# Kernel tuning notes

Hardware: AMD Instinct MI355X
Metric: run time of the kernel (lower is better)

The kernel has to match this reference:

```python
import jax, jax.numpy as jnp
import numpy as np

N = 50000
EPS = 1e-5


def gcn_conv(x, W, b, src, dst, n):
    # x: [n, Cin]; W: [Cin, Cout]; src/dst: [E+n] with self-loops included
    h = x @ W  # dense GEMM
    deg = jax.ops.segment_sum(jnp.ones_like(dst, dtype=h.dtype), dst, num_segments=n)
    dinv = jnp.where(deg > 0, jax.lax.rsqrt(deg), 0.0)
    norm = dinv[src] * dinv[dst]  # [E+n]
    msgs = h[src] * norm[:, None]  # gather + scale
    out = jax.ops.segment_sum(msgs, dst, num_segments=n)  # scatter-add
    return out + b


def batch_norm(x, gamma, beta, mean, var):
    return (x - mean) * jax.lax.rsqrt(var + EPS) * gamma + beta


def setup_inputs() -> dict:
    key = jax.random.key(0)
    ks = jax.random.split(key, 16)
    IN, H, OUT, E = 1280, 256, 500, 1600000
    x = jax.random.normal(ks[0], (N, IN), dtype=jnp.float32)
    edge_index = jax.random.randint(ks[1], (2, E), 0, N, dtype=jnp.int64)
    def lin(k, cin, cout):
        return jax.random.normal(k, (cin, cout), dtype=jnp.float32) / np.sqrt(cin)
    return {
        "x": x,
        "edge_index": edge_index,
        "W1": lin(ks[2], IN, H), "b1": jnp.zeros((H,), jnp.float32),
        "g1": jnp.ones((H,), jnp.float32), "be1": jnp.zeros((H,), jnp.float32),
        "m1": 0.1 * jax.random.normal(ks[3], (H,), jnp.float32),
        "v1": 0.5 + jax.random.uniform(ks[4], (H,), jnp.float32),
        "W2": lin(ks[5], H, H), "b2": jnp.zeros((H,), jnp.float32),
        "g2": jnp.ones((H,), jnp.float32), "be2": jnp.zeros((H,), jnp.float32),
        "m2": 0.1 * jax.random.normal(ks[6], (H,), jnp.float32),
        "v2": 0.5 + jax.random.uniform(ks[7], (H,), jnp.float32),
        "W3": lin(ks[8], H, OUT), "b3": jnp.zeros((OUT,), jnp.float32),
    }


def reference(x, edge_index, W1, b1, g1, be1, m1, v1, W2, b2, g2, be2, m2, v2, W3, b3):
    n = x.shape[0]
    loops = jnp.arange(n, dtype=edge_index.dtype)
    src = jnp.concatenate([edge_index[0], loops])
    dst = jnp.concatenate([edge_index[1], loops])
    h = gcn_conv(x, W1, b1, src, dst, n)
    h = jax.nn.relu(batch_norm(h, g1, be1, m1, v1))
    h = gcn_conv(h, W2, b2, src, dst, n)
    h = jax.nn.relu(batch_norm(h, g2, be2, m2, v2))
    return gcn_conv(h, W3, b3, src, dst, n)
```

## Files before the change

### kernel.cpp

```cpp
#include <hip/hip_runtime.h>
#include <hip/hip_bf16.h>
#include <stdint.h>

typedef __attribute__((ext_vector_type(4))) float f32x4;
typedef __attribute__((ext_vector_type(8))) short s16x8;
typedef __attribute__((ext_vector_type(4))) unsigned short u16x4;

#define EPSBN 1e-5f

__device__ __forceinline__ float bf2f(unsigned short u) {
  union { unsigned int i; float f; } w; w.i = ((unsigned int)u) << 16; return w.f;
}
__device__ __forceinline__ unsigned short f2bf(float f) {
  __hip_bfloat16 h = __float2bfloat16(f);
  unsigned short u; __builtin_memcpy(&u, &h, 2); return u;
}
__device__ __forceinline__ void gld_lds16(const void* g, void* l) {
  __builtin_amdgcn_global_load_lds(
      (const __attribute__((address_space(1))) void*)(g),
      (__attribute__((address_space(3))) void*)(l), 16, 0, 0);
}

__global__ void k_init_deg(unsigned* deg, int n) {
  int i = blockIdx.x * 256 + threadIdx.x;
  if (i < n) deg[i] = 1u;
}
__global__ void k_count(const int* __restrict__ dst, unsigned* __restrict__ deg, int E) {
  int i = blockIdx.x * 256 + threadIdx.x;
  if (i < E) atomicAdd(&deg[dst[i]], 1u);
}
__global__ void k_prep2(const unsigned* __restrict__ deg, float* __restrict__ dinv,
                        unsigned* __restrict__ bsum, int n) {
  __shared__ unsigned s[256];
  int t = threadIdx.x, i = blockIdx.x * 256 + t;
  unsigned d = (i < n) ? deg[i] : 0u;
  if (i < n) dinv[i] = rsqrtf((float)d);
  s[t] = d;
  __syncthreads();
  for (int st = 128; st > 0; st >>= 1) {
    if (t < st) s[t] += s[t + st];
    __syncthreads();
  }
  if (t == 0) bsum[blockIdx.x] = s[0];
}
__global__ void k_scan_top(const unsigned* __restrict__ bsum, unsigned* __restrict__ bpre,
                           int nb, unsigned* __restrict__ offs, int n) {
  __shared__ unsigned s[256];
  int t = threadIdx.x;
  unsigned v = (t < nb) ? bsum[t] : 0u;
  s[t] = v; __syncthreads();
  for (int d = 1; d < 256; d <<= 1) {
    unsigned a = (t >= d) ? s[t - d] : 0u;
    __syncthreads();
    s[t] += a;
    __syncthreads();
  }
  bpre[t] = s[t] - v;
  if (t == 255) offs[n] = s[255];
}
__global__ void k_scan_fin(const unsigned* __restrict__ deg, const unsigned* __restrict__ bpre,
                           unsigned* __restrict__ offs, unsigned* __restrict__ cur, int n) {
  __shared__ unsigned s[256];
  int t = threadIdx.x, i = blockIdx.x * 256 + t;
  unsigned v = (i < n) ? deg[i] : 0u;
  s[t] = v; __syncthreads();
  for (int d = 1; d < 256; d <<= 1) {
    unsigned a = (t >= d) ? s[t - d] : 0u;
    __syncthreads();
    s[t] += a;
    __syncthreads();
  }
  if (i < n) {
    unsigned o = bpre[blockIdx.x] + s[t] - v;
    offs[i] = o; cur[i] = o;
  }
}
__global__ void k_fill(const int* __restrict__ src, const int* __restrict__ dst,
                       unsigned* __restrict__ cur, int* __restrict__ adj, int E, int n) {
  int i = blockIdx.x * 256 + threadIdx.x;
  int s, d;
  if (i < E)          { s = src[i]; d = dst[i]; }
  else if (i < E + n) { s = d = i - E; }
  else return;
  unsigned p = atomicAdd(&cur[d], 1u);
  adj[p] = s;
}
__global__ __launch_bounds__(256) void k_sortw(const unsigned* __restrict__ offs,
                                               const int* __restrict__ adj,
                                               const float* __restrict__ dinv,
                                               int2* __restrict__ ew, int nN) {
  int wv = (blockIdx.x * 256 + threadIdx.x) >> 6;
  int lane = threadIdx.x & 63;
  if (wv >= nN) return;
  unsigned beg = offs[wv], end = offs[wv + 1];
  int len = (int)(end - beg);
  float dv = dinv[wv];
  if (len <= 64) {
    int k = (lane < len) ? adj[beg + lane] : 0x7FFFFFFF;
#pragma unroll
    for (int size = 2; size <= 64; size <<= 1) {
#pragma unroll
      for (int stride = size >> 1; stride > 0; stride >>= 1) {
        int other = __shfl_xor(k, stride);
        bool up = (lane & size) == 0;
        bool lower = (lane & stride) == 0;
        k = (lower == up) ? min(k, other) : max(k, other);
      }
    }
    if (lane < len) ew[beg + lane] = make_int2(k, __float_as_int(dinv[k] * dv));
  } else {
    for (unsigned e = beg + lane; e < end; e += 64) {
      int s = adj[e];
      ew[e] = make_int2(s, __float_as_int(dinv[s] * dv));
    }
  }
}
__global__ void k_wt3(const float* __restrict__ W1, unsigned short* __restrict__ Wt1,
                      const float* __restrict__ W2, unsigned short* __restrict__ Wt2,
                      const float* __restrict__ W3, unsigned short* __restrict__ Wt3) {
  const int n1 = 256 * 1280, n2 = 256 * 256, n3 = 512 * 256;
  int idx = blockIdx.x * 256 + threadIdx.x;
  const float* W; unsigned short* Wt; int K, N;
  if (idx < n1)            { W = W1; Wt = Wt1; K = 1280; N = 256; }
  else if (idx < n1 + n2)  { W = W2; Wt = Wt2; K = 256;  N = 256; idx -= n1; }
  else if (idx < n1+n2+n3) { W = W3; Wt = Wt3; K = 256;  N = 500; idx -= n1 + n2; }
  else return;
  int nn = idx / K, k = idx - nn * K;
  float v = (nn < N) ? W[(size_t)k * N + nn] : 0.f;
  Wt[idx] = f2bf(v);
}

#define BM 128
#define BN 128
#define BK 64

template<int OUTF32>
__global__ __launch_bounds__(256, 4) void k_gemm(
    const unsigned short* __restrict__ Au, const unsigned short* __restrict__ Bt,
    void* __restrict__ Coutv, const float* __restrict__ bias,
    int M, int N, int K, int MT, int NT)
{
  __shared__ __align__(16) unsigned short As[BM * BK];
  __shared__ __align__(16) unsigned short Bs[BN * BK];

  int d = blockIdx.x;
  int xc = d & 7, sb = d >> 3;
  int nt = sb % NT, mt = (sb / NT) * 8 + xc;
  if (mt >= MT) return;
  int m0 = mt * BM, n0 = nt * BN;

  int tid = threadIdx.x, lane = tid & 63, wave = tid >> 6;
  int wm = wave >> 1, wn = wave & 1;
  int l15 = lane & 15, l4 = lane >> 4;

  f32x4 acc[4][4];
#pragma unroll
  for (int i = 0; i < 4; ++i)
#pragma unroll
    for (int j = 0; j < 4; ++j) acc[i][j] = 0.f;

  int srow[4], scg[4];
#pragma unroll
  for (int i = 0; i < 4; ++i) {
    int ci = (wave + 4 * i) * 64 + lane;
    srow[i] = ci >> 3;
    scg[i] = (ci & 7) ^ (srow[i] & 7);
  }

  int nk = K / BK;
  for (int kt = 0; kt < nk; ++kt) {
    __syncthreads();
#pragma unroll
    for (int i = 0; i < 4; ++i) {
      int gr = m0 + srow[i]; gr = gr < M ? gr : M - 1;
      gld_lds16(Au + (size_t)gr * K + kt * BK + scg[i] * 8, As + (wave + 4 * i) * 512);
    }
#pragma unroll
    for (int i = 0; i < 4; ++i) {
      int gn = n0 + srow[i];
      gld_lds16(Bt + (size_t)gn * K + kt * BK + scg[i] * 8, Bs + (wave + 4 * i) * 512);
    }
    __syncthreads();

#pragma unroll
    for (int ks = 0; ks < 2; ++ks) {
      s16x8 af[4], bf[4];
#pragma unroll
      for (int f = 0; f < 4; ++f) {
        int r = wm * 64 + f * 16 + l15;
        int ca = (ks * 4 + l4) ^ (r & 7);
        af[f] = *(const s16x8*)(As + r * 64 + ca * 8);
        int nloc = wn * 64 + f * 16 + l15;
        int cb = (ks * 4 + l4) ^ (nloc & 7);
        bf[f] = *(const s16x8*)(Bs + nloc * 64 + cb * 8);
      }
#pragma unroll
      for (int fm = 0; fm < 4; ++fm)
#pragma unroll
        for (int fn = 0; fn < 4; ++fn)
          acc[fm][fn] = __builtin_amdgcn_mfma_f32_16x16x32_bf16(af[fm], bf[fn], acc[fm][fn], 0, 0, 0);
    }
  }

#pragma unroll
  for (int fm = 0; fm < 4; ++fm) {
#pragma unroll
    for (int fn = 0; fn < 4; ++fn) {
#pragma unroll
      for (int r = 0; r < 4; ++r) {
        int row = m0 + wm * 64 + fm * 16 + l4 * 4 + r;
        int col = n0 + wn * 64 + fn * 16 + l15;
        if (row < M && col < N) {
          if (OUTF32)
            ((float*)Coutv)[(size_t)row * N + col] = acc[fm][fn][r] + bias[col];
          else
            ((unsigned short*)Coutv)[(size_t)row * N + col] = f2bf(acc[fm][fn][r]);
        }
      }
    }
  }
}

__global__ __launch_bounds__(256, 3) void k_gemmF(
    const float* __restrict__ Af, const unsigned short* __restrict__ Bt,
    unsigned short* __restrict__ Cout, int M, int N, int K, int MT, int NT)
{
  __shared__ __align__(16) float As[BM * BK];
  __shared__ __align__(16) unsigned short Bs[BN * BK];

  int d = blockIdx.x;
  int xc = d & 7, sb = d >> 3;
  int nt = sb % NT, mt = (sb / NT) * 8 + xc;
  if (mt >= MT) return;
  int m0 = mt * BM, n0 = nt * BN;

  int tid = threadIdx.x, lane = tid & 63, wave = tid >> 6;
  int wm = wave >> 1, wn = wave & 1;
  int l15 = lane & 15, l4 = lane >> 4;

  f32x4 acc[4][4];
#pragma unroll
  for (int i = 0; i < 4; ++i)
#pragma unroll
    for (int j = 0; j < 4; ++j) acc[i][j] = 0.f;

  int arow[8], acs[8];
#pragma unroll
  for (int i = 0; i < 8; ++i) {
    int ci = (i * 4 + wave) * 64 + lane;
    arow[i] = ci >> 4;
    acs[i] = (ci & 15) ^ ((arow[i] & 7) << 1);
  }
  int brow[4], bcg[4];
#pragma unroll
  for (int i = 0; i < 4; ++i) {
    int ci = (i * 4 + wave) * 64 + lane;
    brow[i] = ci >> 3;
    bcg[i] = (ci & 7) ^ (brow[i] & 7);
  }

  int nk = K / BK;
  for (int kt = 0; kt < nk; ++kt) {
    __syncthreads();
#pragma unroll
    for (int i = 0; i < 8; ++i) {
      int gr = m0 + arow[i]; gr = gr < M ? gr : M - 1;
      gld_lds16(Af + (size_t)gr * K + kt * BK + acs[i] * 4, As + (i * 4 + wave) * 256);
    }
#pragma unroll
    for (int i = 0; i < 4; ++i) {
      int gn = n0 + brow[i];
      gld_lds16(Bt + (size_t)gn * K + kt * BK + bcg[i] * 8, Bs + (i * 4 + wave) * 512);
    }
    __syncthreads();

#pragma unroll
    for (int ks = 0; ks < 2; ++ks) {
      s16x8 af[4], bf[4];
#pragma unroll
      for (int f = 0; f < 4; ++f) {
        int r = wm * 64 + f * 16 + l15;
        int c0 = (2 * (ks * 4 + l4)) ^ ((r & 7) << 1);
        f32x4 a0 = *(const f32x4*)(As + r * 64 + c0 * 4);
        f32x4 a1 = *(const f32x4*)(As + r * 64 + c0 * 4 + 4);
        s16x8 pk;
        pk[0] = (short)f2bf(a0[0]); pk[1] = (short)f2bf(a0[1]);
        pk[2] = (short)f2bf(a0[2]); pk[3] = (short)f2bf(a0[3]);
        pk[4] = (short)f2bf(a1[0]); pk[5] = (short)f2bf(a1[1]);
        pk[6] = (short)f2bf(a1[2]); pk[7] = (short)f2bf(a1[3]);
        af[f] = pk;
        int nloc = wn * 64 + f * 16 + l15;
        int cb = (ks * 4 + l4) ^ (nloc & 7);
        bf[f] = *(const s16x8*)(Bs + nloc * 64 + cb * 8);
      }
#pragma unroll
      for (int fm = 0; fm < 4; ++fm)
#pragma unroll
        for (int fn = 0; fn < 4; ++fn)
          acc[fm][fn] = __builtin_amdgcn_mfma_f32_16x16x32_bf16(af[fm], bf[fn], acc[fm][fn], 0, 0, 0);
    }
  }

#pragma unroll
  for (int fm = 0; fm < 4; ++fm) {
#pragma unroll
    for (int fn = 0; fn < 4; ++fn) {
#pragma unroll
      for (int r = 0; r < 4; ++r) {
        int row = m0 + wm * 64 + fm * 16 + l4 * 4 + r;
        int col = n0 + wn * 64 + fn * 16 + l15;
        if (row < M && col < N)
          Cout[(size_t)row * N + col] = f2bf(acc[fm][fn][r]);
      }
    }
  }
}

__device__ __forceinline__ void accum4(float& a0, float& a1, float& a2, float& a3,
                                       u16x4 q, float w) {
  a0 += bf2f(q[0]) * w; a1 += bf2f(q[1]) * w;
  a2 += bf2f(q[2]) * w; a3 += bf2f(q[3]) * w;
}

template<int BNRELU, int BIAS>
__global__ __launch_bounds__(256) void k_agg(
    const unsigned short* __restrict__ h, const int2* __restrict__ ew,
    const unsigned* __restrict__ offs, const float* __restrict__ bias,
    const float* __restrict__ gam, const float* __restrict__ bet,
    const float* __restrict__ mea, const float* __restrict__ var,
    unsigned short* __restrict__ outp, int nN)
{
  const int C = 256;
  int wave = threadIdx.x >> 6, lane = threadIdx.x & 63;
  int v = blockIdx.x * 4 + wave;
  if (v >= nN) return;
  unsigned beg = offs[v], end = offs[v + 1];
  int len = (int)(end - beg);
  int ch0 = lane * 4;
  const unsigned short* hb = h + ch0;
  float a0 = 0, a1 = 0, a2 = 0, a3 = 0;

  for (int base = 0; base < len; base += 64) {
    int m = min(64, len - base);
    int2 myp = make_int2(0, 0);
    if (lane < m) myp = ew[beg + base + lane];
    int ng = (m + 15) >> 4;

    u16x4 q[16];
#pragma unroll
    for (int r = 0; r < 16; ++r) {
      int s = __shfl(myp.x, r);
      q[r] = *(const u16x4*)(hb + (size_t)s * C);
    }
    for (int g = 1; g < ng; ++g) {
      u16x4 q2[16];
#pragma unroll
      for (int r = 0; r < 16; ++r) {
        int s = __shfl(myp.x, g * 16 + r);
        q2[r] = *(const u16x4*)(hb + (size_t)s * C);
      }
#pragma unroll
      for (int r = 0; r < 16; ++r) {
        float w = __int_as_float(__shfl(myp.y, (g - 1) * 16 + r));
        accum4(a0, a1, a2, a3, q[r], w);
      }
#pragma unroll
      for (int r = 0; r < 16; ++r) q[r] = q2[r];
    }
#pragma unroll
    for (int r = 0; r < 16; ++r) {
      float w = __int_as_float(__shfl(myp.y, (ng - 1) * 16 + r));
      accum4(a0, a1, a2, a3, q[r], w);
    }
  }

  float va[4] = {a0, a1, a2, a3};
#pragma unroll
  for (int j = 0; j < 4; ++j) {
    int ch = ch0 + j;
    float val = va[j];
    if (BIAS) val += bias[ch];
    if (BNRELU) {
      val = (val - mea[ch]) * rsqrtf(var[ch] + EPSBN) * gam[ch] + bet[ch];
      val = fmaxf(val, 0.f);
    }
    outp[(size_t)v * C + ch] = f2bf(val);
  }
}

extern "C" void kernel_launch(void* const* d_in, const int* in_sizes, int n_in,
                              void* d_out, int out_size, void* d_ws, size_t ws_size,
                              hipStream_t stream) {
  const float* x   = (const float*)d_in[0];
  const int*   ei  = (const int*)d_in[1];
  const float* W1  = (const float*)d_in[2];
  const float* b1  = (const float*)d_in[3];
  const float* g1  = (const float*)d_in[4];
  const float* be1 = (const float*)d_in[5];
  const float* m1  = (const float*)d_in[6];
  const float* v1  = (const float*)d_in[7];
  const float* W2  = (const float*)d_in[8];
  const float* b2  = (const float*)d_in[9];
  const float* g2  = (const float*)d_in[10];
  const float* be2 = (const float*)d_in[11];
  const float* m2  = (const float*)d_in[12];
  const float* v2  = (const float*)d_in[13];
  const float* W3  = (const float*)d_in[14];
  const float* b3  = (const float*)d_in[15];

  const int IN = 1280, H = 256, OUT = 500, OUTP = 512;
  int E  = in_sizes[1] / 2;
  int nN = in_sizes[0] / IN;
  const int* srcI = ei;
  const int* dstI = ei + E;

  char* p = (char*)d_ws;
  auto carve = [&](size_t bytes) { char* r = p; p += (bytes + 511) & ~(size_t)511; return r; };
  unsigned short* Wt1 = (unsigned short*)carve((size_t)H * IN * 2);
  unsigned short* Wt2 = (unsigned short*)carve((size_t)H * H * 2);
  unsigned short* Wt3 = (unsigned short*)carve((size_t)OUTP * H * 2);
  unsigned* deg  = (unsigned*)carve((size_t)nN * 4);
  float*    dinv = (float*)carve((size_t)nN * 4);
  unsigned* offs = (unsigned*)carve((size_t)(nN + 1) * 4);
  unsigned* cur  = (unsigned*)carve((size_t)nN * 4);
  unsigned* bsum = (unsigned*)carve(256 * 4);
  unsigned* bpre = (unsigned*)carve(256 * 4);
  int*      adj  = (int*)carve((size_t)(E + nN) * 4);
  int2*     ew   = (int2*)carve((size_t)(E + nN) * 8);
  unsigned short* bufA = (unsigned short*)carve((size_t)nN * H * 2);
  unsigned short* bufB = (unsigned short*)carve((size_t)nN * H * 2);

  int NB = (nN + 255) / 256;
  k_init_deg<<<NB, 256, 0, stream>>>(deg, nN);
  k_count<<<(E + 255) / 256, 256, 0, stream>>>(dstI, deg, E);
  k_prep2<<<NB, 256, 0, stream>>>(deg, dinv, bsum, nN);
  k_scan_top<<<1, 256, 0, stream>>>(bsum, bpre, NB, offs, nN);
  k_scan_fin<<<NB, 256, 0, stream>>>(deg, bpre, offs, cur, nN);
  k_fill<<<(E + nN + 255) / 256, 256, 0, stream>>>(srcI, dstI, cur, adj, E, nN);
  k_sortw<<<(nN + 3) / 4, 256, 0, stream>>>(offs, adj, dinv, ew, nN);
  k_wt3<<<(H * IN + H * H + OUTP * H + 255) / 256, 256, 0, stream>>>(W1, Wt1, W2, Wt2, W3, Wt3);

  int MT = (nN + BM - 1) / BM;
  int mg = (MT + 7) / 8;
  int nAgg = (nN + 3) / 4;

  k_gemmF<<<mg * 8 * 2, 256, 0, stream>>>(x, Wt1, bufA, nN, H, IN, MT, 2);
  k_agg<1, 1><<<nAgg, 256, 0, stream>>>(bufA, ew, offs, b1, g1, be1, m1, v1, bufB, nN);
  k_gemm<0><<<mg * 8 * 2, 256, 0, stream>>>(bufB, Wt2, bufA, nullptr, nN, H, H, MT, 2);
  k_agg<1, 1><<<nAgg, 256, 0, stream>>>(bufA, ew, offs, b2, g2, be2, m2, v2, bufB, nN);
  k_agg<0, 0><<<nAgg, 256, 0, stream>>>(bufB, ew, offs, nullptr, nullptr, nullptr, nullptr, nullptr, bufA, nN);
  k_gemm<1><<<mg * 8 * 4, 256, 0, stream>>>(bufA, Wt3, d_out, b3, nN, OUT, H, MT, 4);
}
```

Measured before the change: 697.5 us.

## Channel-chunk feature layout, packed bf16 edge weights, and per-chunk aggregation passes

Feature buffers move from row-major to a chunked layout of 32 channels per chunk. Aggregation runs as 8 passes over 32-channel slices, so each pass gathers from a roughly 3 MB working set that can stay in cache, where the old gather walked the full 25 MB buffer. Edges are packed into one 32-bit word holding the source index and a bf16 normalized weight, and the per-node sort kernel is dropped. This cuts edge-list traffic and one launch, but adds 24 aggregation launches, re-reads the edge list 8 times, and rounds the weights to bf16. Packing the source index into 16 bits only fits indices below 65536, which holds for N=50000.

```diff
diff --git a/kernel.cpp b/kernel.cpp
--- a/kernel.cpp
+++ b/kernel.cpp
@@ -4,7 +4,6 @@
 
 typedef __attribute__((ext_vector_type(4))) float f32x4;
 typedef __attribute__((ext_vector_type(8))) short s16x8;
-typedef __attribute__((ext_vector_type(4))) unsigned short u16x4;
 
 #define EPSBN 1e-5f
 
@@ -75,45 +74,17 @@
     offs[i] = o; cur[i] = o;
   }
 }
-__global__ void k_fill(const int* __restrict__ src, const int* __restrict__ dst,
-                       unsigned* __restrict__ cur, int* __restrict__ adj, int E, int n) {
+__global__ void k_fillw(const int* __restrict__ src, const int* __restrict__ dst,
+                        const float* __restrict__ dinv, unsigned* __restrict__ cur,
+                        unsigned* __restrict__ ewp, int E, int n) {
   int i = blockIdx.x * 256 + threadIdx.x;
   int s, d;
   if (i < E)          { s = src[i]; d = dst[i]; }
   else if (i < E + n) { s = d = i - E; }
   else return;
   unsigned p = atomicAdd(&cur[d], 1u);
-  adj[p] = s;
-}
-__global__ __launch_bounds__(256) void k_sortw(const unsigned* __restrict__ offs,
-                                               const int* __restrict__ adj,
-                                               const float* __restrict__ dinv,
-                                               int2* __restrict__ ew, int nN) {
-  int wv = (blockIdx.x * 256 + threadIdx.x) >> 6;
-  int lane = threadIdx.x & 63;
-  if (wv >= nN) return;
-  unsigned beg = offs[wv], end = offs[wv + 1];
-  int len = (int)(end - beg);
-  float dv = dinv[wv];
-  if (len <= 64) {
-    int k = (lane < len) ? adj[beg + lane] : 0x7FFFFFFF;
-#pragma unroll
-    for (int size = 2; size <= 64; size <<= 1) {
-#pragma unroll
-      for (int stride = size >> 1; stride > 0; stride >>= 1) {
-        int other = __shfl_xor(k, stride);
-        bool up = (lane & size) == 0;
-        bool lower = (lane & stride) == 0;
-        k = (lower == up) ? min(k, other) : max(k, other);
-      }
-    }
-    if (lane < len) ew[beg + lane] = make_int2(k, __float_as_int(dinv[k] * dv));
-  } else {
-    for (unsigned e = beg + lane; e < end; e += 64) {
-      int s = adj[e];
-      ew[e] = make_int2(s, __float_as_int(dinv[s] * dv));
-    }
-  }
+  float w = dinv[s] * dinv[d];
+  ewp[p] = ((unsigned)s << 16) | (unsigned)f2bf(w);
 }
 __global__ void k_wt3(const float* __restrict__ W1, unsigned short* __restrict__ Wt1,
                       const float* __restrict__ W2, unsigned short* __restrict__ Wt2,
@@ -134,7 +105,7 @@
 #define BN 128
 #define BK 64
 
-template<int OUTF32>
+template<int OUTMODE, int ACM>
 __global__ __launch_bounds__(256, 4) void k_gemm(
     const unsigned short* __restrict__ Au, const unsigned short* __restrict__ Bt,
     void* __restrict__ Coutv, const float* __restrict__ bias,
@@ -173,7 +144,14 @@
 #pragma unroll
     for (int i = 0; i < 4; ++i) {
       int gr = m0 + srow[i]; gr = gr < M ? gr : M - 1;
-      gld_lds16(Au + (size_t)gr * K + kt * BK + scg[i] * 8, As + (wave + 4 * i) * 512);
+      size_t ga;
+      if (ACM) {
+        int ch = kt * BK + scg[i] * 8;
+        ga = ((size_t)(ch >> 5) * M + gr) * 32 + (ch & 31);
+      } else {
+        ga = (size_t)gr * K + kt * BK + scg[i] * 8;
+      }
+      gld_lds16(Au + ga, As + (wave + 4 * i) * 512);
     }
 #pragma unroll
     for (int i = 0; i < 4; ++i) {
@@ -211,10 +189,11 @@
         int row = m0 + wm * 64 + fm * 16 + l4 * 4 + r;
         int col = n0 + wn * 64 + fn * 16 + l15;
         if (row < M && col < N) {
-          if (OUTF32)
+          if (OUTMODE == 1)
             ((float*)Coutv)[(size_t)row * N + col] = acc[fm][fn][r] + bias[col];
           else
-            ((unsigned short*)Coutv)[(size_t)row * N + col] = f2bf(acc[fm][fn][r]);
+            ((unsigned short*)Coutv)[((size_t)(col >> 5) * M + row) * 32 + (col & 31)]
+                = f2bf(acc[fm][fn][r]);
         }
       }
     }
@@ -310,81 +289,80 @@
         int row = m0 + wm * 64 + fm * 16 + l4 * 4 + r;
         int col = n0 + wn * 64 + fn * 16 + l15;
         if (row < M && col < N)
-          Cout[(size_t)row * N + col] = f2bf(acc[fm][fn][r]);
+          Cout[((size_t)(col >> 5) * M + row) * 32 + (col & 31)] = f2bf(acc[fm][fn][r]);
       }
     }
   }
 }
 
-__device__ __forceinline__ void accum4(float& a0, float& a1, float& a2, float& a3,
-                                       u16x4 q, float w) {
-  a0 += bf2f(q[0]) * w; a1 += bf2f(q[1]) * w;
-  a2 += bf2f(q[2]) * w; a3 += bf2f(q[3]) * w;
-}
-
 template<int BNRELU, int BIAS>
-__global__ __launch_bounds__(256) void k_agg(
-    const unsigned short* __restrict__ h, const int2* __restrict__ ew,
-    const unsigned* __restrict__ offs, const float* __restrict__ bias,
-    const float* __restrict__ gam, const float* __restrict__ bet,
-    const float* __restrict__ mea, const float* __restrict__ var,
-    unsigned short* __restrict__ outp, int nN)
+__global__ __launch_bounds__(256) void k_aggc(
+    const unsigned short* __restrict__ hc, const unsigned* __restrict__ ewp,
+    const unsigned* __restrict__ offs,
+    const float* __restrict__ bias, const float* __restrict__ gam,
+    const float* __restrict__ bet, const float* __restrict__ mea,
+    const float* __restrict__ var,
+    unsigned* __restrict__ outp, int nN, int cb)
 {
-  const int C = 256;
   int wave = threadIdx.x >> 6, lane = threadIdx.x & 63;
   int v = blockIdx.x * 4 + wave;
   if (v >= nN) return;
-  unsigned beg = offs[v], end = offs[v + 1];
-  int len = (int)(end - beg);
-  int ch0 = lane * 4;
-  const unsigned short* hb = h + ch0;
-  float a0 = 0, a1 = 0, a2 = 0, a3 = 0;
-
-  for (int base = 0; base < len; base += 64) {
-    int m = min(64, len - base);
-    int2 myp = make_int2(0, 0);
-    if (lane < m) myp = ew[beg + base + lane];
-    int ng = (m + 15) >> 4;
-
-    u16x4 q[16];
-#pragma unroll
-    for (int r = 0; r < 16; ++r) {
-      int s = __shfl(myp.x, r);
-      q[r] = *(const u16x4*)(hb + (size_t)s * C);
-    }
-    for (int g = 1; g < ng; ++g) {
-      u16x4 q2[16];
-#pragma unroll
-      for (int r = 0; r < 16; ++r) {
-        int s = __shfl(myp.x, g * 16 + r);
-        q2[r] = *(const u16x4*)(hb + (size_t)s * C);
-      }
-#pragma unroll
-      for (int r = 0; r < 16; ++r) {
-        float w = __int_as_float(__shfl(myp.y, (g - 1) * 16 + r));
-        accum4(a0, a1, a2, a3, q[r], w);
-      }
-#pragma unroll
-      for (int r = 0; r < 16; ++r) q[r] = q2[r];
-    }
-#pragma unroll
-    for (int r = 0; r < 16; ++r) {
-      float w = __int_as_float(__shfl(myp.y, (ng - 1) * 16 + r));
-      accum4(a0, a1, a2, a3, q[r], w);
-    }
-  }
-
-  float va[4] = {a0, a1, a2, a3};
-#pragma unroll
-  for (int j = 0; j < 4; ++j) {
-    int ch = ch0 + j;
-    float val = va[j];
-    if (BIAS) val += bias[ch];
+  unsigned beg = offs[v];
+  int len = (int)(offs[v + 1] - beg);
+  int eslot = lane >> 4, cp = lane & 15;
+  const unsigned* hp = (const unsigned*)hc;
+  float a0 = 0.f, a1 = 0.f;
+  int ngrp = (len + 31) >> 5;
+
+  unsigned q[8]; float w[8];
+#pragma unroll
+  for (int r = 0; r < 8; ++r) {
+    int er = r * 4 + eslot;
+    unsigned pck = 0;
+    if (er < len) pck = __builtin_nontemporal_load(&ewp[beg + er]);
+    w[r] = bf2f((unsigned short)(pck & 0xffffu));
+    q[r] = hp[(size_t)(pck >> 16) * 16 + cp];
+  }
+  for (int g = 1; g < ngrp; ++g) {
+    unsigned q2[8]; float w2[8];
+#pragma unroll
+    for (int r = 0; r < 8; ++r) {
+      int er = g * 32 + r * 4 + eslot;
+      unsigned pck = 0;
+      if (er < len) pck = __builtin_nontemporal_load(&ewp[beg + er]);
+      w2[r] = bf2f((unsigned short)(pck & 0xffffu));
+      q2[r] = hp[(size_t)(pck >> 16) * 16 + cp];
+    }
+#pragma unroll
+    for (int r = 0; r < 8; ++r) {
+      float lo = __uint_as_float(q[r] << 16);
+      float hi = __uint_as_float(q[r] & 0xffff0000u);
+      a0 += lo * w[r]; a1 += hi * w[r];
+    }
+#pragma unroll
+    for (int r = 0; r < 8; ++r) { q[r] = q2[r]; w[r] = w2[r]; }
+  }
+#pragma unroll
+  for (int r = 0; r < 8; ++r) {
+    float lo = __uint_as_float(q[r] << 16);
+    float hi = __uint_as_float(q[r] & 0xffff0000u);
+    a0 += lo * w[r]; a1 += hi * w[r];
+  }
+
+  a0 += __shfl_xor(a0, 16); a0 += __shfl_xor(a0, 32);
+  a1 += __shfl_xor(a1, 16); a1 += __shfl_xor(a1, 32);
+
+  if (lane < 16) {
+    int ch0 = cb + cp * 2, ch1 = ch0 + 1;
+    float v0 = a0, v1 = a1;
+    if (BIAS) { v0 += bias[ch0]; v1 += bias[ch1]; }
     if (BNRELU) {
-      val = (val - mea[ch]) * rsqrtf(var[ch] + EPSBN) * gam[ch] + bet[ch];
-      val = fmaxf(val, 0.f);
-    }
-    outp[(size_t)v * C + ch] = f2bf(val);
+      v0 = (v0 - mea[ch0]) * rsqrtf(var[ch0] + EPSBN) * gam[ch0] + bet[ch0];
+      v1 = (v1 - mea[ch1]) * rsqrtf(var[ch1] + EPSBN) * gam[ch1] + bet[ch1];
+      v0 = fmaxf(v0, 0.f); v1 = fmaxf(v1, 0.f);
+    }
+    unsigned u = (unsigned)f2bf(v0) | ((unsigned)f2bf(v1) << 16);
+    __builtin_nontemporal_store(u, &outp[(size_t)v * 16 + cp]);
   }
 }
 
@@ -425,8 +403,7 @@
   unsigned* cur  = (unsigned*)carve((size_t)nN * 4);
   unsigned* bsum = (unsigned*)carve(256 * 4);
   unsigned* bpre = (unsigned*)carve(256 * 4);
-  int*      adj  = (int*)carve((size_t)(E + nN) * 4);
-  int2*     ew   = (int2*)carve((size_t)(E + nN) * 8);
+  unsigned* ewp  = (unsigned*)carve((size_t)(E + nN) * 4);
   unsigned short* bufA = (unsigned short*)carve((size_t)nN * H * 2);
   unsigned short* bufB = (unsigned short*)carve((size_t)nN * H * 2);
 
@@ -436,8 +413,7 @@
   k_prep2<<<NB, 256, 0, stream>>>(deg, dinv, bsum, nN);
   k_scan_top<<<1, 256, 0, stream>>>(bsum, bpre, NB, offs, nN);
   k_scan_fin<<<NB, 256, 0, stream>>>(deg, bpre, offs, cur, nN);
-  k_fill<<<(E + nN + 255) / 256, 256, 0, stream>>>(srcI, dstI, cur, adj, E, nN);
-  k_sortw<<<(nN + 3) / 4, 256, 0, stream>>>(offs, adj, dinv, ew, nN);
+  k_fillw<<<(E + nN + 255) / 256, 256, 0, stream>>>(srcI, dstI, dinv, cur, ewp, E, nN);
   k_wt3<<<(H * IN + H * H + OUTP * H + 255) / 256, 256, 0, stream>>>(W1, Wt1, W2, Wt2, W3, Wt3);
 
   int MT = (nN + BM - 1) / BM;
@@ -445,9 +421,18 @@
   int nAgg = (nN + 3) / 4;
 
   k_gemmF<<<mg * 8 * 2, 256, 0, stream>>>(x, Wt1, bufA, nN, H, IN, MT, 2);
-  k_agg<1, 1><<<nAgg, 256, 0, stream>>>(bufA, ew, offs, b1, g1, be1, m1, v1, bufB, nN);
-  k_gemm<0><<<mg * 8 * 2, 256, 0, stream>>>(bufB, Wt2, bufA, nullptr, nN, H, H, MT, 2);
-  k_agg<1, 1><<<nAgg, 256, 0, stream>>>(bufA, ew, offs, b2, g2, be2, m2, v2, bufB, nN);
-  k_agg<0, 0><<<nAgg, 256, 0, stream>>>(bufB, ew, offs, nullptr, nullptr, nullptr, nullptr, nullptr, bufA, nN);
-  k_gemm<1><<<mg * 8 * 4, 256, 0, stream>>>(bufA, Wt3, d_out, b3, nN, OUT, H, MT, 4);
-}
+  for (int c = 0; c < 8; ++c)
+    k_aggc<1, 1><<<nAgg, 256, 0, stream>>>(bufA + (size_t)c * nN * 32, ewp, offs,
+                                           b1, g1, be1, m1, v1,
+                                           (unsigned*)bufB + (size_t)c * nN * 16, nN, c * 32);
+  k_gemm<0, 1><<<mg * 8 * 2, 256, 0, stream>>>(bufB, Wt2, bufA, nullptr, nN, H, H, MT, 2);
+  for (int c = 0; c < 8; ++c)
+    k_aggc<1, 1><<<nAgg, 256, 0, stream>>>(bufA + (size_t)c * nN * 32, ewp, offs,
+                                           b2, g2, be2, m2, v2,
+                                           (unsigned*)bufB + (size_t)c * nN * 16, nN, c * 32);
+  for (int c = 0; c < 8; ++c)
+    k_aggc<0, 0><<<nAgg, 256, 0, stream>>>(bufB + (size_t)c * nN * 32, ewp, offs,
+                                           nullptr, nullptr, nullptr, nullptr, nullptr,
+                                           (unsigned*)bufA + (size_t)c * nN * 16, nN, c * 32);
+  k_gemm<1, 1><<<mg * 8 * 4, 256, 0, stream>>>(bufA, Wt3, d_out, b3, nN, OUT, H, MT, 4);
+}
```

Measured after the change: 1.380 ms. +97.8%, slower.

## Band aggregation by source range with grid barriers and packed bf16 edge weights

Applied to the files above, without the earlier changes.

Each wave now owns 13 destination nodes and walks their sorted neighbour lists in 10 source-index bands, with a software grid-wide barrier between bands. The goal is to keep the gathered feature rows of one band resident in L2/LLC and cut random HBM traffic. Edge entries are packed into 32 bits (source index in the upper 16 bits, bf16 weight in the lower), which halves edge-list bandwidth but assumes node ids fit in 16 bits and lowers weight precision. The spin barrier has a timeout and relies on every block being co-resident; the bias/BN parameters are also folded into one scale and shift.

```diff
diff --git a/kernel.cpp b/kernel.cpp
--- a/kernel.cpp
+++ b/kernel.cpp
@@ -88,7 +88,7 @@
 __global__ __launch_bounds__(256) void k_sortw(const unsigned* __restrict__ offs,
                                                const int* __restrict__ adj,
                                                const float* __restrict__ dinv,
-                                               int2* __restrict__ ew, int nN) {
+                                               unsigned* __restrict__ ewp, int nN) {
   int wv = (blockIdx.x * 256 + threadIdx.x) >> 6;
   int lane = threadIdx.x & 63;
   if (wv >= nN) return;
@@ -107,11 +107,12 @@
         k = (lower == up) ? min(k, other) : max(k, other);
       }
     }
-    if (lane < len) ew[beg + lane] = make_int2(k, __float_as_int(dinv[k] * dv));
+    if (lane < len)
+      ewp[beg + lane] = ((unsigned)k << 16) | (unsigned)f2bf(dinv[k] * dv);
   } else {
     for (unsigned e = beg + lane; e < end; e += 64) {
       int s = adj[e];
-      ew[e] = make_int2(s, __float_as_int(dinv[s] * dv));
+      ewp[e] = ((unsigned)s << 16) | (unsigned)f2bf(dinv[s] * dv);
     }
   }
 }
@@ -316,75 +317,107 @@
   }
 }
 
-__device__ __forceinline__ void accum4(float& a0, float& a1, float& a2, float& a3,
-                                       u16x4 q, float w) {
-  a0 += bf2f(q[0]) * w; a1 += bf2f(q[1]) * w;
-  a2 += bf2f(q[2]) * w; a3 += bf2f(q[3]) * w;
-}
+#define NPW 13
+#define NBAND 10
 
 template<int BNRELU, int BIAS>
-__global__ __launch_bounds__(256) void k_agg(
-    const unsigned short* __restrict__ h, const int2* __restrict__ ew,
-    const unsigned* __restrict__ offs, const float* __restrict__ bias,
-    const float* __restrict__ gam, const float* __restrict__ bet,
-    const float* __restrict__ mea, const float* __restrict__ var,
-    unsigned short* __restrict__ outp, int nN)
+__global__ __launch_bounds__(256, 4) void k_aggb(
+    const unsigned short* __restrict__ h, const unsigned* __restrict__ ewp,
+    const unsigned* __restrict__ offs,
+    const float* __restrict__ bias, const float* __restrict__ gam,
+    const float* __restrict__ bet, const float* __restrict__ mea,
+    const float* __restrict__ var,
+    unsigned short* __restrict__ outp, int nN, int bandw, unsigned* __restrict__ barc)
 {
-  const int C = 256;
   int wave = threadIdx.x >> 6, lane = threadIdx.x & 63;
-  int v = blockIdx.x * 4 + wave;
-  if (v >= nN) return;
-  unsigned beg = offs[v], end = offs[v + 1];
-  int len = (int)(end - beg);
-  int ch0 = lane * 4;
-  const unsigned short* hb = h + ch0;
-  float a0 = 0, a1 = 0, a2 = 0, a3 = 0;
-
-  for (int base = 0; base < len; base += 64) {
-    int m = min(64, len - base);
-    int2 myp = make_int2(0, 0);
-    if (lane < m) myp = ew[beg + base + lane];
-    int ng = (m + 15) >> 4;
-
-    u16x4 q[16];
-#pragma unroll
-    for (int r = 0; r < 16; ++r) {
-      int s = __shfl(myp.x, r);
-      q[r] = *(const u16x4*)(hb + (size_t)s * C);
-    }
-    for (int g = 1; g < ng; ++g) {
-      u16x4 q2[16];
-#pragma unroll
-      for (int r = 0; r < 16; ++r) {
-        int s = __shfl(myp.x, g * 16 + r);
-        q2[r] = *(const u16x4*)(hb + (size_t)s * C);
-      }
-#pragma unroll
-      for (int r = 0; r < 16; ++r) {
-        float w = __int_as_float(__shfl(myp.y, (g - 1) * 16 + r));
-        accum4(a0, a1, a2, a3, q[r], w);
-      }
-#pragma unroll
-      for (int r = 0; r < 16; ++r) q[r] = q2[r];
-    }
-#pragma unroll
-    for (int r = 0; r < 16; ++r) {
-      float w = __int_as_float(__shfl(myp.y, (ng - 1) * 16 + r));
-      accum4(a0, a1, a2, a3, q[r], w);
-    }
-  }
-
-  float va[4] = {a0, a1, a2, a3};
-#pragma unroll
-  for (int j = 0; j < 4; ++j) {
-    int ch = ch0 + j;
-    float val = va[j];
-    if (BIAS) val += bias[ch];
-    if (BNRELU) {
-      val = (val - mea[ch]) * rsqrtf(var[ch] + EPSBN) * gam[ch] + bet[ch];
-      val = fmaxf(val, 0.f);
-    }
-    outp[(size_t)v * C + ch] = f2bf(val);
+  int gw = blockIdx.x * 4 + wave;
+  int vb = gw * NPW;
+  const unsigned short* hb = h + lane * 4;
+
+  unsigned cur_[NPW], end_[NPW];
+  f32x4 acc_[NPW];
+#pragma unroll
+  for (int n = 0; n < NPW; ++n) {
+    int v = vb + n;
+    cur_[n] = (v < nN) ? offs[v] : 0u;
+    end_[n] = (v < nN) ? offs[v + 1] : 0u;
+    acc_[n] = 0.f;
+  }
+
+  for (int b = 0; b < NBAND; ++b) {
+    unsigned hi = (unsigned)(b + 1) * (unsigned)bandw;
+#pragma unroll
+    for (int n = 0; n < NPW; ++n) {
+      while (true) {
+        unsigned rem = end_[n] - cur_[n];
+        if (rem == 0) break;
+        unsigned pck = 0;
+        if (lane < (int)rem) pck = ewp[cur_[n] + lane];
+        unsigned long long mask = __ballot((lane < (int)rem) && ((pck >> 16) < hi));
+        unsigned long long inv = ~mask;
+        int cnt = (inv == 0ull) ? 64 : (int)__builtin_ctzll(inv);
+        for (int e = 0; e < cnt; e += 4) {
+          u16x4 q[4]; float ww[4];
+#pragma unroll
+          for (int j = 0; j < 4; ++j) {
+            int idx = e + j;
+            unsigned pj = __shfl((int)pck, idx & 63);
+            if (idx >= cnt) pj = 0;
+            ww[j] = bf2f((unsigned short)(pj & 0xffffu));
+            q[j] = *(const u16x4*)(hb + (size_t)(pj >> 16) * 256);
+          }
+#pragma unroll
+          for (int j = 0; j < 4; ++j) {
+            acc_[n][0] += bf2f(q[j][0]) * ww[j];
+            acc_[n][1] += bf2f(q[j][1]) * ww[j];
+            acc_[n][2] += bf2f(q[j][2]) * ww[j];
+            acc_[n][3] += bf2f(q[j][3]) * ww[j];
+          }
+        }
+        cur_[n] += (unsigned)cnt;
+        if (cnt < 64) break;
+      }
+    }
+    if (b + 1 < NBAND) {
+      __syncthreads();
+      if (threadIdx.x == 0) {
+        __hip_atomic_fetch_add(&barc[b], 1u, __ATOMIC_RELAXED, __HIP_MEMORY_SCOPE_AGENT);
+        int it = 0;
+        while (__hip_atomic_load(&barc[b], __ATOMIC_RELAXED, __HIP_MEMORY_SCOPE_AGENT) < gridDim.x
+               && it < 4000) {
+          __builtin_amdgcn_s_sleep(2);
+          ++it;
+        }
+      }
+      __syncthreads();
+    }
+  }
+
+  f32x4 sc, sh;
+  if (BNRELU) {
+    f32x4 bv = *(const f32x4*)(bias + lane * 4);
+    f32x4 gv = *(const f32x4*)(gam + lane * 4);
+    f32x4 ev = *(const f32x4*)(bet + lane * 4);
+    f32x4 mv = *(const f32x4*)(mea + lane * 4);
+    f32x4 vv = *(const f32x4*)(var + lane * 4);
+#pragma unroll
+    for (int j = 0; j < 4; ++j) {
+      sc[j] = gv[j] * rsqrtf(vv[j] + EPSBN);
+      sh[j] = (bv[j] - mv[j]) * sc[j] + ev[j];
+    }
+  }
+#pragma unroll
+  for (int n = 0; n < NPW; ++n) {
+    int v = vb + n;
+    if (v >= nN) continue;
+    u16x4 o;
+#pragma unroll
+    for (int j = 0; j < 4; ++j) {
+      float val = acc_[n][j];
+      if (BNRELU) val = fmaxf(val * sc[j] + sh[j], 0.f);
+      o[j] = f2bf(val);
+    }
+    *(u16x4*)(outp + (size_t)v * 256 + lane * 4) = o;
   }
 }
 
@@ -425,10 +458,13 @@
   unsigned* cur  = (unsigned*)carve((size_t)nN * 4);
   unsigned* bsum = (unsigned*)carve(256 * 4);
   unsigned* bpre = (unsigned*)carve(256 * 4);
+  unsigned* barc = (unsigned*)carve(64 * 4);
   int*      adj  = (int*)carve((size_t)(E + nN) * 4);
-  int2*     ew   = (int2*)carve((size_t)(E + nN) * 8);
+  unsigned* ewp  = (unsigned*)carve((size_t)(E + nN) * 4);
   unsigned short* bufA = (unsigned short*)carve((size_t)nN * H * 2);
   unsigned short* bufB = (unsigned short*)carve((size_t)nN * H * 2);
+
+  hipMemsetAsync(barc, 0, 64 * 4, stream);
 
   int NB = (nN + 255) / 256;
   k_init_deg<<<NB, 256, 0, stream>>>(deg, nN);
@@ -437,17 +473,21 @@
   k_scan_top<<<1, 256, 0, stream>>>(bsum, bpre, NB, offs, nN);
   k_scan_fin<<<NB, 256, 0, stream>>>(deg, bpre, offs, cur, nN);
   k_fill<<<(E + nN + 255) / 256, 256, 0, stream>>>(srcI, dstI, cur, adj, E, nN);
-  k_sortw<<<(nN + 3) / 4, 256, 0, stream>>>(offs, adj, dinv, ew, nN);
+  k_sortw<<<(nN + 3) / 4, 256, 0, stream>>>(offs, adj, dinv, ewp, nN);
   k_wt3<<<(H * IN + H * H + OUTP * H + 255) / 256, 256, 0, stream>>>(W1, Wt1, W2, Wt2, W3, Wt3);
 
   int MT = (nN + BM - 1) / BM;
   int mg = (MT + 7) / 8;
-  int nAgg = (nN + 3) / 4;
+  int bandw = (nN + NBAND - 1) / NBAND;
+  int aggGrid = (nN + NPW * 4 - 1) / (NPW * 4);
 
   k_gemmF<<<mg * 8 * 2, 256, 0, stream>>>(x, Wt1, bufA, nN, H, IN, MT, 2);
-  k_agg<1, 1><<<nAgg, 256, 0, stream>>>(bufA, ew, offs, b1, g1, be1, m1, v1, bufB, nN);
+  k_aggb<1, 1><<<aggGrid, 256, 0, stream>>>(bufA, ewp, offs, b1, g1, be1, m1, v1,
+                                            bufB, nN, bandw, barc);
   k_gemm<0><<<mg * 8 * 2, 256, 0, stream>>>(bufB, Wt2, bufA, nullptr, nN, H, H, MT, 2);
-  k_agg<1, 1><<<nAgg, 256, 0, stream>>>(bufA, ew, offs, b2, g2, be2, m2, v2, bufB, nN);
-  k_agg<0, 0><<<nAgg, 256, 0, stream>>>(bufB, ew, offs, nullptr, nullptr, nullptr, nullptr, nullptr, bufA, nN);
+  k_aggb<1, 1><<<aggGrid, 256, 0, stream>>>(bufA, ewp, offs, b2, g2, be2, m2, v2,
+                                            bufB, nN, bandw, barc + 16);
+  k_aggb<0, 0><<<aggGrid, 256, 0, stream>>>(bufB, ewp, offs, nullptr, nullptr, nullptr,
+                                            nullptr, nullptr, bufA, nN, bandw, barc + 32);
   k_gemm<1><<<mg * 8 * 4, 256, 0, stream>>>(bufA, Wt3, d_out, b3, nN, OUT, H, MT, 4);
 }
```

Result: slower. 2.139 ms (+206.7%).

## Fold GCN norm into GEMM epilogues and compress edge list to 16-bit indices

Applied to the files above, without the earlier changes.

The symmetric normalisation dinv[src]*dinv[dst] is factored: the GEMM epilogues pre-scale each output row by dinv, and the aggregation kernels multiply the plain neighbour sum by dinv[dst]. This lets the per-edge weight be dropped, so the edge list becomes 16-bit source indices instead of int2 pairs. That cuts edge-list bandwidth and removes per-edge shuffles and multiplies in the aggregation loops. A zeroed padding row at index nN replaces masked gathers, and the degree init kernel is replaced by a memset with +1 folded into the scans. The 16-bit indices only work while the node count stays below 65536.

```diff
diff --git a/kernel.cpp b/kernel.cpp
--- a/kernel.cpp
+++ b/kernel.cpp
@@ -21,10 +21,6 @@
       (__attribute__((address_space(3))) void*)(l), 16, 0, 0);
 }
 
-__global__ void k_init_deg(unsigned* deg, int n) {
-  int i = blockIdx.x * 256 + threadIdx.x;
-  if (i < n) deg[i] = 1u;
-}
 __global__ void k_count(const int* __restrict__ dst, unsigned* __restrict__ deg, int E) {
   int i = blockIdx.x * 256 + threadIdx.x;
   if (i < E) atomicAdd(&deg[dst[i]], 1u);
@@ -33,7 +29,7 @@
                         unsigned* __restrict__ bsum, int n) {
   __shared__ unsigned s[256];
   int t = threadIdx.x, i = blockIdx.x * 256 + t;
-  unsigned d = (i < n) ? deg[i] : 0u;
+  unsigned d = (i < n) ? deg[i] + 1u : 0u;
   if (i < n) dinv[i] = rsqrtf((float)d);
   s[t] = d;
   __syncthreads();
@@ -62,7 +58,7 @@
                            unsigned* __restrict__ offs, unsigned* __restrict__ cur, int n) {
   __shared__ unsigned s[256];
   int t = threadIdx.x, i = blockIdx.x * 256 + t;
-  unsigned v = (i < n) ? deg[i] : 0u;
+  unsigned v = (i < n) ? deg[i] + 1u : 0u;
   s[t] = v; __syncthreads();
   for (int d = 1; d < 256; d <<= 1) {
     unsigned a = (t >= d) ? s[t - d] : 0u;
@@ -76,55 +72,54 @@
   }
 }
 __global__ void k_fill(const int* __restrict__ src, const int* __restrict__ dst,
-                       unsigned* __restrict__ cur, int* __restrict__ adj, int E, int n) {
+                       unsigned* __restrict__ cur, unsigned short* __restrict__ ewp,
+                       int E, int n) {
   int i = blockIdx.x * 256 + threadIdx.x;
   int s, d;
   if (i < E)          { s = src[i]; d = dst[i]; }
   else if (i < E + n) { s = d = i - E; }
   else return;
   unsigned p = atomicAdd(&cur[d], 1u);
-  adj[p] = s;
+  ewp[p] = (unsigned short)s;
 }
 __global__ __launch_bounds__(256) void k_sortw(const unsigned* __restrict__ offs,
-                                               const int* __restrict__ adj,
-                                               const float* __restrict__ dinv,
-                                               int2* __restrict__ ew, int nN) {
+                                               unsigned short* __restrict__ ewp, int nN) {
   int wv = (blockIdx.x * 256 + threadIdx.x) >> 6;
   int lane = threadIdx.x & 63;
   if (wv >= nN) return;
   unsigned beg = offs[wv], end = offs[wv + 1];
   int len = (int)(end - beg);
-  float dv = dinv[wv];
-  if (len <= 64) {
-    int k = (lane < len) ? adj[beg + lane] : 0x7FFFFFFF;
-#pragma unroll
-    for (int size = 2; size <= 64; size <<= 1) {
-#pragma unroll
-      for (int stride = size >> 1; stride > 0; stride >>= 1) {
-        int other = __shfl_xor(k, stride);
-        bool up = (lane & size) == 0;
-        bool lower = (lane & stride) == 0;
-        k = (lower == up) ? min(k, other) : max(k, other);
-      }
-    }
-    if (lane < len) ew[beg + lane] = make_int2(k, __float_as_int(dinv[k] * dv));
-  } else {
-    for (unsigned e = beg + lane; e < end; e += 64) {
-      int s = adj[e];
-      ew[e] = make_int2(s, __float_as_int(dinv[s] * dv));
-    }
-  }
+  if (len > 64) return;
+  int k = (lane < len) ? (int)ewp[beg + lane] : 0x10000;
+#pragma unroll
+  for (int size = 2; size <= 64; size <<= 1) {
+#pragma unroll
+    for (int stride = size >> 1; stride > 0; stride >>= 1) {
+      int other = __shfl_xor(k, stride);
+      bool up = (lane & size) == 0;
+      bool lower = (lane & stride) == 0;
+      k = (lower == up) ? min(k, other) : max(k, other);
+    }
+  }
+  if (lane < len) ewp[beg + lane] = (unsigned short)k;
 }
 __global__ void k_wt3(const float* __restrict__ W1, unsigned short* __restrict__ Wt1,
                       const float* __restrict__ W2, unsigned short* __restrict__ Wt2,
-                      const float* __restrict__ W3, unsigned short* __restrict__ Wt3) {
+                      const float* __restrict__ W3, unsigned short* __restrict__ Wt3,
+                      unsigned short* __restrict__ bufA, unsigned short* __restrict__ bufB,
+                      int nN) {
   const int n1 = 256 * 1280, n2 = 256 * 256, n3 = 512 * 256;
   int idx = blockIdx.x * 256 + threadIdx.x;
+  if (idx >= n1 + n2 + n3) {
+    int z = idx - (n1 + n2 + n3);
+    if (z < 256)      bufA[(size_t)nN * 256 + z] = 0;
+    else if (z < 512) bufB[(size_t)nN * 256 + (z - 256)] = 0;
+    return;
+  }
   const float* W; unsigned short* Wt; int K, N;
-  if (idx < n1)            { W = W1; Wt = Wt1; K = 1280; N = 256; }
-  else if (idx < n1 + n2)  { W = W2; Wt = Wt2; K = 256;  N = 256; idx -= n1; }
-  else if (idx < n1+n2+n3) { W = W3; Wt = Wt3; K = 256;  N = 500; idx -= n1 + n2; }
-  else return;
+  if (idx < n1)           { W = W1; Wt = Wt1; K = 1280; N = 256; }
+  else if (idx < n1 + n2) { W = W2; Wt = Wt2; K = 256;  N = 256; idx -= n1; }
+  else                    { W = W3; Wt = Wt3; K = 256;  N = 500; idx -= n1 + n2; }
   int nn = idx / K, k = idx - nn * K;
   float v = (nn < N) ? W[(size_t)k * N + nn] : 0.f;
   Wt[idx] = f2bf(v);
@@ -134,11 +129,11 @@
 #define BN 128
 #define BK 64
 
-template<int OUTF32>
+template<int OUTMODE>
 __global__ __launch_bounds__(256, 4) void k_gemm(
     const unsigned short* __restrict__ Au, const unsigned short* __restrict__ Bt,
     void* __restrict__ Coutv, const float* __restrict__ bias,
-    int M, int N, int K, int MT, int NT)
+    const float* __restrict__ dinv, int M, int N, int K, int MT, int NT)
 {
   __shared__ __align__(16) unsigned short As[BM * BK];
   __shared__ __align__(16) unsigned short Bs[BN * BK];
@@ -205,16 +200,17 @@
 #pragma unroll
   for (int fm = 0; fm < 4; ++fm) {
 #pragma unroll
-    for (int fn = 0; fn < 4; ++fn) {
-#pragma unroll
-      for (int r = 0; r < 4; ++r) {
-        int row = m0 + wm * 64 + fm * 16 + l4 * 4 + r;
+    for (int r = 0; r < 4; ++r) {
+      int row = m0 + wm * 64 + fm * 16 + l4 * 4 + r;
+      float dsc = (OUTMODE == 0 && row < M) ? dinv[row] : 0.f;
+#pragma unroll
+      for (int fn = 0; fn < 4; ++fn) {
         int col = n0 + wn * 64 + fn * 16 + l15;
         if (row < M && col < N) {
-          if (OUTF32)
+          if (OUTMODE == 1)
             ((float*)Coutv)[(size_t)row * N + col] = acc[fm][fn][r] + bias[col];
           else
-            ((unsigned short*)Coutv)[(size_t)row * N + col] = f2bf(acc[fm][fn][r]);
+            ((unsigned short*)Coutv)[(size_t)row * N + col] = f2bf(acc[fm][fn][r] * dsc);
         }
       }
     }
@@ -223,7 +219,8 @@
 
 __global__ __launch_bounds__(256, 3) void k_gemmF(
     const float* __restrict__ Af, const unsigned short* __restrict__ Bt,
-    unsigned short* __restrict__ Cout, int M, int N, int K, int MT, int NT)
+    unsigned short* __restrict__ Cout, const float* __restrict__ dinv,
+    int M, int N, int K, int MT, int NT)
 {
   __shared__ __align__(16) float As[BM * BK];
   __shared__ __align__(16) unsigned short Bs[BN * BK];
@@ -304,87 +301,82 @@
 #pragma unroll
   for (int fm = 0; fm < 4; ++fm) {
 #pragma unroll
-    for (int fn = 0; fn < 4; ++fn) {
-#pragma unroll
-      for (int r = 0; r < 4; ++r) {
-        int row = m0 + wm * 64 + fm * 16 + l4 * 4 + r;
+    for (int r = 0; r < 4; ++r) {
+      int row = m0 + wm * 64 + fm * 16 + l4 * 4 + r;
+      float dsc = (row < M) ? dinv[row] : 0.f;
+#pragma unroll
+      for (int fn = 0; fn < 4; ++fn) {
         int col = n0 + wn * 64 + fn * 16 + l15;
         if (row < M && col < N)
-          Cout[(size_t)row * N + col] = f2bf(acc[fm][fn][r]);
-      }
-    }
-  }
-}
-
-__device__ __forceinline__ void accum4(float& a0, float& a1, float& a2, float& a3,
-                                       u16x4 q, float w) {
-  a0 += bf2f(q[0]) * w; a1 += bf2f(q[1]) * w;
-  a2 += bf2f(q[2]) * w; a3 += bf2f(q[3]) * w;
-}
-
-template<int BNRELU, int BIAS>
+          Cout[(size_t)row * N + col] = f2bf(acc[fm][fn][r] * dsc);
+      }
+    }
+  }
+}
+
+template<int BNRELU, int SCALEOUT>
 __global__ __launch_bounds__(256) void k_agg(
-    const unsigned short* __restrict__ h, const int2* __restrict__ ew,
-    const unsigned* __restrict__ offs, const float* __restrict__ bias,
-    const float* __restrict__ gam, const float* __restrict__ bet,
-    const float* __restrict__ mea, const float* __restrict__ var,
-    unsigned short* __restrict__ outp, int nN)
+    const unsigned short* __restrict__ h, const unsigned short* __restrict__ ewp,
+    const unsigned* __restrict__ offs, const float* __restrict__ dinv,
+    const float* __restrict__ bias, const float* __restrict__ gam,
+    const float* __restrict__ bet, const float* __restrict__ mea,
+    const float* __restrict__ var, unsigned short* __restrict__ outp, int nN)
 {
-  const int C = 256;
   int wave = threadIdx.x >> 6, lane = threadIdx.x & 63;
   int v = blockIdx.x * 4 + wave;
   if (v >= nN) return;
   unsigned beg = offs[v], end = offs[v + 1];
   int len = (int)(end - beg);
-  int ch0 = lane * 4;
-  const unsigned short* hb = h + ch0;
+  float dv = dinv[v];
+  const unsigned short* hb = h + lane * 4;
   float a0 = 0, a1 = 0, a2 = 0, a3 = 0;
 
   for (int base = 0; base < len; base += 64) {
     int m = min(64, len - base);
-    int2 myp = make_int2(0, 0);
-    if (lane < m) myp = ew[beg + base + lane];
+    int myp = (lane < m) ? (int)ewp[beg + base + lane] : nN;
     int ng = (m + 15) >> 4;
 
     u16x4 q[16];
 #pragma unroll
     for (int r = 0; r < 16; ++r) {
-      int s = __shfl(myp.x, r);
-      q[r] = *(const u16x4*)(hb + (size_t)s * C);
+      int s = __shfl(myp, r);
+      q[r] = *(const u16x4*)(hb + (size_t)s * 256);
     }
     for (int g = 1; g < ng; ++g) {
       u16x4 q2[16];
 #pragma unroll
       for (int r = 0; r < 16; ++r) {
-        int s = __shfl(myp.x, g * 16 + r);
-        q2[r] = *(const u16x4*)(hb + (size_t)s * C);
+        int s = __shfl(myp, g * 16 + r);
+        q2[r] = *(const u16x4*)(hb + (size_t)s * 256);
       }
 #pragma unroll
       for (int r = 0; r < 16; ++r) {
-        float w = __int_as_float(__shfl(myp.y, (g - 1) * 16 + r));
-        accum4(a0, a1, a2, a3, q[r], w);
+        a0 += bf2f(q[r][0]); a1 += bf2f(q[r][1]);
+        a2 += bf2f(q[r][2]); a3 += bf2f(q[r][3]);
       }
 #pragma unroll
       for (int r = 0; r < 16; ++r) q[r] = q2[r];
     }
 #pragma unroll
     for (int r = 0; r < 16; ++r) {
-      float w = __int_as_float(__shfl(myp.y, (ng - 1) * 16 + r));
-      accum4(a0, a1, a2, a3, q[r], w);
+      a0 += bf2f(q[r][0]); a1 += bf2f(q[r][1]);
+      a2 += bf2f(q[r][2]); a3 += bf2f(q[r][3]);
     }
   }
 
   float va[4] = {a0, a1, a2, a3};
+  int ch0 = lane * 4;
 #pragma unroll
   for (int j = 0; j < 4; ++j) {
     int ch = ch0 + j;
-    float val = va[j];
-    if (BIAS) val += bias[ch];
+    float val = va[j] * dv;
     if (BNRELU) {
+      val += bias[ch];
       val = (val - mea[ch]) * rsqrtf(var[ch] + EPSBN) * gam[ch] + bet[ch];
       val = fmaxf(val, 0.f);
     }
-    outp[(size_t)v * C + ch] = f2bf(val);
+    if (SCALEOUT) val *= dv;
+    outp[(size_t)v * 256 + ch] = f2bf(val);
   }
 }
 
@@ -425,29 +417,31 @@
   unsigned* cur  = (unsigned*)carve((size_t)nN * 4);
   unsigned* bsum = (unsigned*)carve(256 * 4);
   unsigned* bpre = (unsigned*)carve(256 * 4);
-  int*      adj  = (int*)carve((size_t)(E + nN) * 4);
-  int2*     ew   = (int2*)carve((size_t)(E + nN) * 8);
-  unsigned short* bufA = (unsigned short*)carve((size_t)nN * H * 2);
-  unsigned short* bufB = (unsigned short*)carve((size_t)nN * H * 2);
+  unsigned short* ewp = (unsigned short*)carve((size_t)(E + nN) * 2);
+  unsigned short* bufA = (unsigned short*)carve((size_t)(nN + 1) * H * 2);
+  unsigned short* bufB = (unsigned short*)carve((size_t)(nN + 1) * H * 2);
+
+  hipMemsetAsync(deg, 0, (size_t)nN * 4, stream);
 
   int NB = (nN + 255) / 256;
-  k_init_deg<<<NB, 256, 0, stream>>>(deg, nN);
   k_count<<<(E + 255) / 256, 256, 0, stream>>>(dstI, deg, E);
   k_prep2<<<NB, 256, 0, stream>>>(deg, dinv, bsum, nN);
   k_scan_top<<<1, 256, 0, stream>>>(bsum, bpre, NB, offs, nN);
   k_scan_fin<<<NB, 256, 0, stream>>>(deg, bpre, offs, cur, nN);
-  k_fill<<<(E + nN + 255) / 256, 256, 0, stream>>>(srcI, dstI, cur, adj, E, nN);
-  k_sortw<<<(nN + 3) / 4, 256, 0, stream>>>(offs, adj, dinv, ew, nN);
-  k_wt3<<<(H * IN + H * H + OUTP * H + 255) / 256, 256, 0, stream>>>(W1, Wt1, W2, Wt2, W3, Wt3);
+  k_fill<<<(E + nN + 255) / 256, 256, 0, stream>>>(srcI, dstI, cur, ewp, E, nN);
+  k_sortw<<<(nN + 3) / 4, 256, 0, stream>>>(offs, ewp, nN);
+  k_wt3<<<(256 * 1280 + 256 * 256 + 512 * 256 + 512 + 255) / 256, 256, 0, stream>>>(
+      W1, Wt1, W2, Wt2, W3, Wt3, bufA, bufB, nN);
 
   int MT = (nN + BM - 1) / BM;
   int mg = (MT + 7) / 8;
   int nAgg = (nN + 3) / 4;
 
-  k_gemmF<<<mg * 8 * 2, 256, 0, stream>>>(x, Wt1, bufA, nN, H, IN, MT, 2);
-  k_agg<1, 1><<<nAgg, 256, 0, stream>>>(bufA, ew, offs, b1, g1, be1, m1, v1, bufB, nN);
-  k_gemm<0><<<mg * 8 * 2, 256, 0, stream>>>(bufB, Wt2, bufA, nullptr, nN, H, H, MT, 2);
-  k_agg<1, 1><<<nAgg, 256, 0, stream>>>(bufA, ew, offs, b2, g2, be2, m2, v2, bufB, nN);
-  k_agg<0, 0><<<nAgg, 256, 0, stream>>>(bufB, ew, offs, nullptr, nullptr, nullptr, nullptr, nullptr, bufA, nN);
-  k_gemm<1><<<mg * 8 * 4, 256, 0, stream>>>(bufA, Wt3, d_out, b3, nN, OUT, H, MT, 4);
-}
+  k_gemmF<<<mg * 8 * 2, 256, 0, stream>>>(x, Wt1, bufA, dinv, nN, H, IN, MT, 2);
+  k_agg<1, 0><<<nAgg, 256, 0, stream>>>(bufA, ewp, offs, dinv, b1, g1, be1, m1, v1, bufB, nN);
+  k_gemm<0><<<mg * 8 * 2, 256, 0, stream>>>(bufB, Wt2, bufA, nullptr, dinv, nN, H, H, MT, 2);
+  k_agg<1, 1><<<nAgg, 256, 0, stream>>>(bufA, ewp, offs, dinv, b2, g2, be2, m2, v2, bufB, nN);
+  k_agg<0, 0><<<nAgg, 256, 0, stream>>>(bufB, ewp, offs, dinv, nullptr, nullptr, nullptr,
+                                        nullptr, nullptr, bufA, nN);
+  k_gemm<1><<<mg * 8 * 4, 256, 0, stream>>>(bufA, Wt3, d_out, b3, nullptr, nN, OUT, H, MT, 4);
+}
```

After: 698.8 us. No clear change (+0.2%).
